# Optimization experiments

Hardware: AMD Instinct MI355X
Metric: run time of the kernel (lower is better)

The kernel has to match this reference:

```python
import jax, jax.numpy as jnp
import numpy as np

N_NODES = 50000
N_EDGES = 1000000
D = 64
L = 3
BN_EPS = 1e-5


def setup_inputs() -> dict:
    key = jax.random.key(0)
    ks = jax.random.split(key, 6)
    x = jax.random.normal(ks[0], (N_NODES, D), dtype=jnp.float32)
    edge_src = jax.random.randint(ks[1], (N_EDGES,), 0, N_NODES)
    edge_dst = jax.random.randint(ks[2], (N_EDGES,), 0, N_NODES)
    edge_weight = jax.random.uniform(ks[3], (N_EDGES,), dtype=jnp.float32)
    W = jax.random.normal(ks[4], (L, D, D), dtype=jnp.float32) * (1.0 / np.sqrt(D))
    b = jnp.zeros((L, D), dtype=jnp.float32)
    prelu_a = jnp.full((L,), 0.25, dtype=jnp.float32)  # torch PReLU default init
    bn_gamma = jnp.ones((L, D), dtype=jnp.float32)
    bn_beta = jnp.zeros((L, D), dtype=jnp.float32)
    return {"x": x, "edge_src": edge_src, "edge_dst": edge_dst,
            "edge_weight": edge_weight, "W": W, "b": b, "prelu_a": prelu_a,
            "bn_gamma": bn_gamma, "bn_beta": bn_beta}


def reference(x, edge_src, edge_dst, edge_weight, W, b, prelu_a, bn_gamma, bn_beta):
    n = x.shape[0]
    h = x
    for i in range(L):
        h_in = h
        # GCNConv (normalize=False): aggregate edge_weight * (h @ W)[src] at dst, + bias
        xw = h @ W[i]                                       # [N, D]
        msg = edge_weight[:, None] * xw[edge_src]            # [E, D] gather
        agg = jax.ops.segment_sum(msg, edge_dst, num_segments=n) + b[i]
        # PReLU (single shared parameter per module)
        h = jnp.where(agg >= 0, agg, prelu_a[i] * agg)
        if i > 0:
            h = h + h_in
        # BatchNorm1d, training-mode batch statistics over nodes
        mean = jnp.mean(h, axis=0)
        var = jnp.mean((h - mean) ** 2, axis=0)  # biased variance, as torch BN
        h = bn_gamma[i] * (h - mean) * jax.lax.rsqrt(var + BN_EPS) + bn_beta[i]
        # dropout p=0.0 -> identity
    return h
```

## Files before the change

### kernel.cpp

```cpp
#include <hip/hip_runtime.h>
#include <hip/hip_fp16.h>

#define N_NODES 50000
#define N_EDGES 1000000
#define D 64
#define L 3
#define BN_EPS 1e-5f
#define NB_SCAN ((N_NODES + 255) / 256)
#define AGG_BLOCKS 1024

__device__ inline void bn_affine(const float* __restrict__ bnsum,
                                 const float* __restrict__ gamma,
                                 const float* __restrict__ beta,
                                 int c, float& sc, float& sh) {
    float mean = bnsum[c] * (1.f / N_NODES);
    float var = fmaf(-mean, mean, bnsum[D + c] * (1.f / N_NODES));
    float inv = rsqrtf(var + BN_EPS);
    sc = gamma[c] * inv;
    sh = fmaf(-mean, sc, beta[c]);
}

__device__ inline float unpack_w(unsigned int m) {
    __half_raw hr;
    hr.x = (unsigned short)(m & 0xffffu);
    __half h = *reinterpret_cast<__half*>(&hr);
    return __half2float(h);
}

__device__ inline float2 unpack_x2(unsigned int q) {
    __half2 h2 = *reinterpret_cast<__half2*>(&q);
    return __half22float2(h2);
}

__device__ inline float2 ntload_f2(const float2* p) {
    unsigned long long u = __builtin_nontemporal_load((const unsigned long long*)p);
    float2 r;
    r.x = __uint_as_float((unsigned int)(u & 0xffffffffull));
    r.y = __uint_as_float((unsigned int)(u >> 32));
    return r;
}

__device__ inline void ntstore_f2(float2* p, float2 v) {
    unsigned long long u =
        ((unsigned long long)__float_as_uint(v.y) << 32) | (unsigned long long)__float_as_uint(v.x);
    __builtin_nontemporal_store(u, (unsigned long long*)p);
}

__global__ void init_kernel(int* __restrict__ counts, float* __restrict__ bnsum) {
    int i = blockIdx.x * blockDim.x + threadIdx.x;
    int stride = gridDim.x * blockDim.x;
    for (int j = i; j < N_NODES; j += stride) counts[j] = 0;
    for (int j = i; j < L * 2 * D; j += stride) bnsum[j] = 0.f;
}

__global__ void count_kernel(const int* __restrict__ dst, int* __restrict__ counts,
                             unsigned short* __restrict__ rank) {
    int i = blockIdx.x * blockDim.x + threadIdx.x;
    int stride = gridDim.x * blockDim.x;
    for (int e = i; e < N_EDGES; e += stride) {
        int r = atomicAdd(&counts[dst[e]], 1);
        rank[e] = (unsigned short)r;
    }
}

__global__ __launch_bounds__(256) void scanA_kernel(const int* __restrict__ counts,
                                                    int* __restrict__ blocksum) {
    __shared__ int buf[256];
    int t = threadIdx.x, b = blockIdx.x;
    int i = b * 256 + t;
    int v = (i < N_NODES) ? counts[i] : 0;
    buf[t] = v;
    __syncthreads();
    for (int off = 128; off > 0; off >>= 1) {
        if (t < off) buf[t] += buf[t + off];
        __syncthreads();
    }
    if (t == 0) blocksum[b] = buf[0];
}

__global__ __launch_bounds__(256) void scanB_kernel(const int* __restrict__ blocksum,
                                                    int* __restrict__ blockoff,
                                                    int* __restrict__ row_ptr) {
    __shared__ int buf[256];
    int t = threadIdx.x;
    int v = (t < NB_SCAN) ? blocksum[t] : 0;
    buf[t] = v;
    __syncthreads();
    for (int off = 1; off < 256; off <<= 1) {
        int u = (t >= off) ? buf[t - off] : 0;
        __syncthreads();
        buf[t] += u;
        __syncthreads();
    }
    if (t < NB_SCAN) blockoff[t] = buf[t] - v;
    if (t == NB_SCAN - 1) row_ptr[N_NODES] = buf[t];
}

__global__ __launch_bounds__(256) void scanC_kernel(const int* __restrict__ counts,
                                                    const int* __restrict__ blockoff,
                                                    int* __restrict__ row_ptr) {
    __shared__ int buf[256];
    int t = threadIdx.x, b = blockIdx.x;
    int i = b * 256 + t;
    int v = (i < N_NODES) ? counts[i] : 0;
    buf[t] = v;
    __syncthreads();
    for (int off = 1; off < 256; off <<= 1) {
        int u = (t >= off) ? buf[t - off] : 0;
        __syncthreads();
        buf[t] += u;
        __syncthreads();
    }
    if (i < N_NODES) row_ptr[i] = blockoff[b] + buf[t] - v;
}

__global__ void fill_kernel(const int* __restrict__ src, const int* __restrict__ dst,
                            const float* __restrict__ w,
                            const unsigned short* __restrict__ rank,
                            const int* __restrict__ row_ptr,
                            unsigned int* __restrict__ em) {
    int i = blockIdx.x * blockDim.x + threadIdx.x;
    int stride = gridDim.x * blockDim.x;
    for (int e = i; e < N_EDGES; e += stride) {
        int d = dst[e];
        int p = row_ptr[d] + (int)rank[e];
        __half h = __float2half_rn(w[e]);
        unsigned short wb = reinterpret_cast<__half_raw*>(&h)->x;
        em[p] = ((unsigned int)src[e] << 16) | (unsigned int)wb;
    }
}

__global__ __launch_bounds__(256) void gemm_kernel(const float* __restrict__ hraw,
                                                   const float* __restrict__ bnsum_p,
                                                   const float* __restrict__ gamma_p,
                                                   const float* __restrict__ beta_p,
                                                   const float* __restrict__ Wl,
                                                   __half* __restrict__ xw) {
    __shared__ float aff[2][D];
    int tid = threadIdx.x, lane = tid & 63, wave = tid >> 6;
    if (tid < D) {
        float sc = 1.f, sh = 0.f;
        if (bnsum_p) bn_affine(bnsum_p, gamma_p, beta_p, tid, sc, sh);
        aff[0][tid] = sc;
        aff[1][tid] = sh;
    }
    __syncthreads();
    float Wreg[D];
    float biasc = 0.f;
#pragma unroll
    for (int k = 0; k < D; k++) {
        float wkc = Wl[k * D + lane];
        biasc = fmaf(aff[1][k], wkc, biasc);
        Wreg[k] = wkc * aff[0][k];
    }
    int gw = blockIdx.x * 4 + wave, nw = gridDim.x * 4;
    for (int v = gw; v < N_NODES; v += nw) {
        const float* hp = hraw + (size_t)__builtin_amdgcn_readfirstlane(v) * D;
        float acc = biasc;
#pragma unroll
        for (int k = 0; k < D; k++) acc = fmaf(hp[k], Wreg[k], acc);
        xw[v * D + lane] = __float2half_rn(acc);
    }
}

__global__ __launch_bounds__(256) void agg_kernel(const uint2* __restrict__ xw,
                                                  const int* __restrict__ row_ptr,
                                                  const unsigned int* __restrict__ em,
                                                  const float* __restrict__ bl,
                                                  const float* __restrict__ pa,
                                                  const float* __restrict__ hraw_prev,
                                                  const float* __restrict__ bnsum_p,
                                                  const float* __restrict__ gamma_p,
                                                  const float* __restrict__ beta_p,
                                                  float* __restrict__ hpre,
                                                  float* __restrict__ bnsum) {
    __shared__ float r1[D], r2[D];
    int tid = threadIdx.x, lane = tid & 63;
    int sub = tid >> 4;
    int fl = lane & 15;
    int srcbase = lane & 48;
    if (tid < D) { r1[tid] = 0.f; r2[tid] = 0.f; }
    __syncthreads();

    float al = pa[0];
    int c0 = 4 * fl;
    float4 bias = ((const float4*)bl)[fl];
    float sc0 = 0, sc1 = 0, sc2 = 0, sc3 = 0, sh0 = 0, sh1 = 0, sh2 = 0, sh3 = 0;
    if (hraw_prev) {
        bn_affine(bnsum_p, gamma_p, beta_p, c0 + 0, sc0, sh0);
        bn_affine(bnsum_p, gamma_p, beta_p, c0 + 1, sc1, sh1);
        bn_affine(bnsum_p, gamma_p, beta_p, c0 + 2, sc2, sh2);
        bn_affine(bnsum_p, gamma_p, beta_p, c0 + 3, sc3, sh3);
    }
    float t1_0 = 0, t1_1 = 0, t1_2 = 0, t1_3 = 0;
    float t2_0 = 0, t2_1 = 0, t2_2 = 0, t2_3 = 0;

    for (int v = blockIdx.x * 16 + sub; v < N_NODES; v += gridDim.x * 16) {
        int e0 = row_ptr[v], e1 = row_ptr[v + 1];
        float a0 = 0, a1 = 0, a2 = 0, a3 = 0, b0 = 0, b1 = 0, b2 = 0, b3 = 0;
        for (int e = e0; e < e1; e += 16) {
            unsigned mo = (e + fl < e1) ? __builtin_nontemporal_load(em + e + fl) : 0u;
            unsigned mj[16];
            uint2 q[16];
#pragma unroll
            for (int j = 0; j < 16; j++) {
                mj[j] = (unsigned)__shfl((int)mo, srcbase + j, 64);
                q[j] = xw[(mj[j] >> 16) * 16 + fl];
            }
#pragma unroll
            for (int j = 0; j < 16; j++) {
                float w = unpack_w(mj[j]);
                float2 f01 = unpack_x2(q[j].x);
                float2 f23 = unpack_x2(q[j].y);
                if (j & 1) {
                    b0 = fmaf(w, f01.x, b0); b1 = fmaf(w, f01.y, b1);
                    b2 = fmaf(w, f23.x, b2); b3 = fmaf(w, f23.y, b3);
                } else {
                    a0 = fmaf(w, f01.x, a0); a1 = fmaf(w, f01.y, a1);
                    a2 = fmaf(w, f23.x, a2); a3 = fmaf(w, f23.y, a3);
                }
            }
        }
        float h0 = a0 + b0 + bias.x;
        float h1 = a1 + b1 + bias.y;
        float h2 = a2 + b2 + bias.z;
        float h3 = a3 + b3 + bias.w;
        h0 = h0 >= 0.f ? h0 : al * h0;
        h1 = h1 >= 0.f ? h1 : al * h1;
        h2 = h2 >= 0.f ? h2 : al * h2;
        h3 = h3 >= 0.f ? h3 : al * h3;
        if (hraw_prev) {
            float2 p01 = ntload_f2((const float2*)hraw_prev + v * 32 + 2 * fl);
            float2 p23 = ntload_f2((const float2*)hraw_prev + v * 32 + 2 * fl + 1);
            h0 = fmaf(p01.x, sc0, h0 + sh0);
            h1 = fmaf(p01.y, sc1, h1 + sh1);
            h2 = fmaf(p23.x, sc2, h2 + sh2);
            h3 = fmaf(p23.y, sc3, h3 + sh3);
        }
        ntstore_f2((float2*)hpre + v * 32 + 2 * fl, make_float2(h0, h1));
        ntstore_f2((float2*)hpre + v * 32 + 2 * fl + 1, make_float2(h2, h3));
        t1_0 += h0; t1_1 += h1; t1_2 += h2; t1_3 += h3;
        t2_0 = fmaf(h0, h0, t2_0);
        t2_1 = fmaf(h1, h1, t2_1);
        t2_2 = fmaf(h2, h2, t2_2);
        t2_3 = fmaf(h3, h3, t2_3);
    }
    atomicAdd(&r1[c0 + 0], t1_0);
    atomicAdd(&r1[c0 + 1], t1_1);
    atomicAdd(&r1[c0 + 2], t1_2);
    atomicAdd(&r1[c0 + 3], t1_3);
    atomicAdd(&r2[c0 + 0], t2_0);
    atomicAdd(&r2[c0 + 1], t2_1);
    atomicAdd(&r2[c0 + 2], t2_2);
    atomicAdd(&r2[c0 + 3], t2_3);
    __syncthreads();
    if (tid < D) {
        atomicAdd(&bnsum[tid], r1[tid]);
        atomicAdd(&bnsum[D + tid], r2[tid]);
    }
}

__global__ __launch_bounds__(256) void bnapply_kernel(const float* __restrict__ hpre,
                                                      const float* __restrict__ bnsum_p,
                                                      const float* __restrict__ gamma_p,
                                                      const float* __restrict__ beta_p,
                                                      float* __restrict__ out) {
    __shared__ float aff[2][D];
    int tid = threadIdx.x;
    if (tid < D) {
        float sc, sh;
        bn_affine(bnsum_p, gamma_p, beta_p, tid, sc, sh);
        aff[0][tid] = sc;
        aff[1][tid] = sh;
    }
    __syncthreads();
    int i = blockIdx.x * blockDim.x + tid;
    int stride = gridDim.x * blockDim.x;
    const int NQ = N_NODES * D / 4;
    for (int j = i; j < NQ; j += stride) {
        float4 hv = ((const float4*)hpre)[j];
        int c = (j * 4) & 63;
        float4 o;
        o.x = fmaf(hv.x, aff[0][c + 0], aff[1][c + 0]);
        o.y = fmaf(hv.y, aff[0][c + 1], aff[1][c + 1]);
        o.z = fmaf(hv.z, aff[0][c + 2], aff[1][c + 2]);
        o.w = fmaf(hv.w, aff[0][c + 3], aff[1][c + 3]);
        ((float4*)out)[j] = o;
    }
}

extern "C" void kernel_launch(void* const* d_in, const int* in_sizes, int n_in,
                              void* d_out, int out_size, void* d_ws, size_t ws_size,
                              hipStream_t stream) {
    const float* x     = (const float*)d_in[0];
    const int*   esrc  = (const int*)d_in[1];
    const int*   edst  = (const int*)d_in[2];
    const float* ew    = (const float*)d_in[3];
    const float* W     = (const float*)d_in[4];
    const float* b     = (const float*)d_in[5];
    const float* pa    = (const float*)d_in[6];
    const float* gamma = (const float*)d_in[7];
    const float* beta  = (const float*)d_in[8];
    float* out = (float*)d_out;

    char* ws = (char*)d_ws;
    size_t off = 0;
    auto alloc = [&](size_t bytes) -> char* {
        char* p = ws + off;
        off = (off + bytes + 255) & ~(size_t)255;
        return p;
    };
    int*            counts   = (int*)alloc((size_t)N_NODES * 4);
    int*            row_ptr  = (int*)alloc((size_t)(N_NODES + 1) * 4);
    int*            blocksum = (int*)alloc((size_t)NB_SCAN * 4);
    int*            blockoff = (int*)alloc((size_t)NB_SCAN * 4);
    unsigned short* rank     = (unsigned short*)alloc((size_t)N_EDGES * 2);
    unsigned int*   em       = (unsigned int*)alloc((size_t)N_EDGES * 4);
    __half*         xw       = (__half*)alloc((size_t)N_NODES * D * 2);
    float*          hpre1    = (float*)alloc((size_t)N_NODES * D * 4);
    float*          bnsum    = (float*)alloc((size_t)L * 2 * D * 4);

    init_kernel<<<256, 256, 0, stream>>>(counts, bnsum);
    count_kernel<<<2048, 256, 0, stream>>>(edst, counts, rank);
    scanA_kernel<<<NB_SCAN, 256, 0, stream>>>(counts, blocksum);
    scanB_kernel<<<1, 256, 0, stream>>>(blocksum, blockoff, row_ptr);
    scanC_kernel<<<NB_SCAN, 256, 0, stream>>>(counts, blockoff, row_ptr);
    fill_kernel<<<2048, 256, 0, stream>>>(esrc, edst, ew, rank, row_ptr, em);

    float* hbuf[L] = {out, hpre1, out};
    for (int i = 0; i < L; i++) {
        const float* hin = (i == 0) ? x : hbuf[i - 1];
        const float* bns = (i == 0) ? nullptr : bnsum + (i - 1) * 2 * D;
        const float* gmp = (i == 0) ? nullptr : gamma + (i - 1) * D;
        const float* btp = (i == 0) ? nullptr : beta + (i - 1) * D;
        gemm_kernel<<<512, 256, 0, stream>>>(hin, bns, gmp, btp, W + (size_t)i * D * D, xw);
        agg_kernel<<<AGG_BLOCKS, 256, 0, stream>>>((const uint2*)xw, row_ptr, em,
                                                   b + i * D, pa + i,
                                                   (i == 0) ? nullptr : hbuf[i - 1],
                                                   bns, gmp, btp,
                                                   hbuf[i], bnsum + i * 2 * D);
    }
    bnapply_kernel<<<2048, 256, 0, stream>>>(hbuf[2], bnsum + 2 * 2 * D,
                                             gamma + 2 * D, beta + 2 * D, out);
}
```

Before: 278.3 us.

## Privatize degree counting per XCD and unroll aggregation to 32 edges

Degree counting now uses a separate counter array per XCD, selected from the hardware XCC id, so atomics stay local to one die's L2. A new kernel turns the per-XCD counts into per-XCD offsets, and the fill pass uses an XCD id packed into the rank field. The aggregation kernel now launches one node per 16-lane group, with no grid-stride loop, and loads 32 edges per iteration to increase gather parallelism. The rank encoding assumes each per-XCD degree fits in 13 bits, and the change adds an extra kernel plus more memory traffic for eight copies of the counts.

Result: slower. 415.5 us (+49.3%).

```diff
diff --git a/kernel.cpp b/kernel.cpp
--- a/kernel.cpp
+++ b/kernel.cpp
@@ -7,7 +7,14 @@
 #define L 3
 #define BN_EPS 1e-5f
 #define NB_SCAN ((N_NODES + 255) / 256)
-#define AGG_BLOCKS 1024
+#define AGG_BLOCKS ((N_NODES + 15) / 16)
+#define NXCD 8
+
+__device__ inline int get_xcc() {
+    int x;
+    asm volatile("s_getreg_b32 %0, hwreg(HW_REG_XCC_ID)" : "=s"(x));
+    return x & (NXCD - 1);
+}
 
 __device__ inline void bn_affine(const float* __restrict__ bnsum,
                                  const float* __restrict__ gamma,
@@ -46,29 +53,37 @@
     __builtin_nontemporal_store(u, (unsigned long long*)p);
 }
 
-__global__ void init_kernel(int* __restrict__ counts, float* __restrict__ bnsum) {
+__global__ void init_kernel(int* __restrict__ counts8, float* __restrict__ bnsum) {
     int i = blockIdx.x * blockDim.x + threadIdx.x;
     int stride = gridDim.x * blockDim.x;
-    for (int j = i; j < N_NODES; j += stride) counts[j] = 0;
+    for (int j = i; j < NXCD * N_NODES; j += stride) counts8[j] = 0;
     for (int j = i; j < L * 2 * D; j += stride) bnsum[j] = 0.f;
 }
 
-__global__ void count_kernel(const int* __restrict__ dst, int* __restrict__ counts,
-                             unsigned short* __restrict__ rank) {
+__global__ void count_kernel(const int* __restrict__ dst, int* __restrict__ counts8,
+                             unsigned short* __restrict__ rankx) {
+    int xcd = get_xcc();
+    int* mycnt = counts8 + (size_t)xcd * N_NODES;
     int i = blockIdx.x * blockDim.x + threadIdx.x;
     int stride = gridDim.x * blockDim.x;
     for (int e = i; e < N_EDGES; e += stride) {
-        int r = atomicAdd(&counts[dst[e]], 1);
-        rank[e] = (unsigned short)r;
-    }
-}
-
-__global__ __launch_bounds__(256) void scanA_kernel(const int* __restrict__ counts,
+        int r = atomicAdd(&mycnt[dst[e]], 1);
+        rankx[e] = (unsigned short)(r | (xcd << 13));
+    }
+}
+
+__global__ __launch_bounds__(256) void scanA_kernel(const int* __restrict__ counts8,
+                                                    int* __restrict__ counts,
                                                     int* __restrict__ blocksum) {
     __shared__ int buf[256];
     int t = threadIdx.x, b = blockIdx.x;
     int i = b * 256 + t;
-    int v = (i < N_NODES) ? counts[i] : 0;
+    int v = 0;
+    if (i < N_NODES) {
+#pragma unroll
+        for (int x = 0; x < NXCD; x++) v += counts8[(size_t)x * N_NODES + i];
+        counts[i] = v;
+    }
     buf[t] = v;
     __syncthreads();
     for (int off = 128; off > 0; off >>= 1) {
@@ -114,16 +129,31 @@
     if (i < N_NODES) row_ptr[i] = blockoff[b] + buf[t] - v;
 }
 
+__global__ __launch_bounds__(256) void offs8_kernel(const int* __restrict__ counts8,
+                                                    const int* __restrict__ row_ptr,
+                                                    int* __restrict__ offs8) {
+    int i = blockIdx.x * blockDim.x + threadIdx.x;
+    if (i < N_NODES) {
+        int base = row_ptr[i];
+#pragma unroll
+        for (int x = 0; x < NXCD; x++) {
+            offs8[(size_t)x * N_NODES + i] = base;
+            base += counts8[(size_t)x * N_NODES + i];
+        }
+    }
+}
+
 __global__ void fill_kernel(const int* __restrict__ src, const int* __restrict__ dst,
                             const float* __restrict__ w,
-                            const unsigned short* __restrict__ rank,
-                            const int* __restrict__ row_ptr,
+                            const unsigned short* __restrict__ rankx,
+                            const int* __restrict__ offs8,
                             unsigned int* __restrict__ em) {
     int i = blockIdx.x * blockDim.x + threadIdx.x;
     int stride = gridDim.x * blockDim.x;
     for (int e = i; e < N_EDGES; e += stride) {
         int d = dst[e];
-        int p = row_ptr[d] + (int)rank[e];
+        unsigned rx = rankx[e];
+        int p = offs8[(size_t)(rx >> 13) * N_NODES + d] + (int)(rx & 0x1fffu);
         __half h = __float2half_rn(w[e]);
         unsigned short wb = reinterpret_cast<__half_raw*>(&h)->x;
         em[p] = ((unsigned int)src[e] << 16) | (unsigned int)wb;
@@ -195,21 +225,28 @@
     float t1_0 = 0, t1_1 = 0, t1_2 = 0, t1_3 = 0;
     float t2_0 = 0, t2_1 = 0, t2_2 = 0, t2_3 = 0;
 
-    for (int v = blockIdx.x * 16 + sub; v < N_NODES; v += gridDim.x * 16) {
+    int v = blockIdx.x * 16 + sub;
+    if (v < N_NODES) {
         int e0 = row_ptr[v], e1 = row_ptr[v + 1];
         float a0 = 0, a1 = 0, a2 = 0, a3 = 0, b0 = 0, b1 = 0, b2 = 0, b3 = 0;
-        for (int e = e0; e < e1; e += 16) {
-            unsigned mo = (e + fl < e1) ? __builtin_nontemporal_load(em + e + fl) : 0u;
-            unsigned mj[16];
-            uint2 q[16];
+        for (int e = e0; e < e1; e += 32) {
+            unsigned mlo = (e + fl < e1) ? __builtin_nontemporal_load(em + e + fl) : 0u;
+            unsigned mhi = (e + 16 + fl < e1) ? __builtin_nontemporal_load(em + e + 16 + fl) : 0u;
+            uint2 q[32];
 #pragma unroll
             for (int j = 0; j < 16; j++) {
-                mj[j] = (unsigned)__shfl((int)mo, srcbase + j, 64);
-                q[j] = xw[(mj[j] >> 16) * 16 + fl];
+                unsigned m = (unsigned)__shfl((int)mlo, srcbase + j, 64);
+                q[j] = xw[(m >> 16) * 16 + fl];
             }
 #pragma unroll
             for (int j = 0; j < 16; j++) {
-                float w = unpack_w(mj[j]);
+                unsigned m = (unsigned)__shfl((int)mhi, srcbase + j, 64);
+                q[16 + j] = xw[(m >> 16) * 16 + fl];
+            }
+#pragma unroll
+            for (int j = 0; j < 32; j++) {
+                unsigned m = (unsigned)__shfl((int)(j < 16 ? mlo : mhi), srcbase + (j & 15), 64);
+                float w = unpack_w(m);
                 float2 f01 = unpack_x2(q[j].x);
                 float2 f23 = unpack_x2(q[j].y);
                 if (j & 1) {
@@ -239,11 +276,8 @@
         }
         ntstore_f2((float2*)hpre + v * 32 + 2 * fl, make_float2(h0, h1));
         ntstore_f2((float2*)hpre + v * 32 + 2 * fl + 1, make_float2(h2, h3));
-        t1_0 += h0; t1_1 += h1; t1_2 += h2; t1_3 += h3;
-        t2_0 = fmaf(h0, h0, t2_0);
-        t2_1 = fmaf(h1, h1, t2_1);
-        t2_2 = fmaf(h2, h2, t2_2);
-        t2_3 = fmaf(h3, h3, t2_3);
+        t1_0 = h0; t1_1 = h1; t1_2 = h2; t1_3 = h3;
+        t2_0 = h0 * h0; t2_1 = h1 * h1; t2_2 = h2 * h2; t2_3 = h3 * h3;
     }
     atomicAdd(&r1[c0 + 0], t1_0);
     atomicAdd(&r1[c0 + 1], t1_1);
@@ -310,22 +344,25 @@
         off = (off + bytes + 255) & ~(size_t)255;
         return p;
     };
+    int*            counts8  = (int*)alloc((size_t)NXCD * N_NODES * 4);
     int*            counts   = (int*)alloc((size_t)N_NODES * 4);
     int*            row_ptr  = (int*)alloc((size_t)(N_NODES + 1) * 4);
+    int*            offs8    = (int*)alloc((size_t)NXCD * N_NODES * 4);
     int*            blocksum = (int*)alloc((size_t)NB_SCAN * 4);
     int*            blockoff = (int*)alloc((size_t)NB_SCAN * 4);
-    unsigned short* rank     = (unsigned short*)alloc((size_t)N_EDGES * 2);
+    unsigned short* rankx    = (unsigned short*)alloc((size_t)N_EDGES * 2);
     unsigned int*   em       = (unsigned int*)alloc((size_t)N_EDGES * 4);
     __half*         xw       = (__half*)alloc((size_t)N_NODES * D * 2);
     float*          hpre1    = (float*)alloc((size_t)N_NODES * D * 4);
     float*          bnsum    = (float*)alloc((size_t)L * 2 * D * 4);
 
-    init_kernel<<<256, 256, 0, stream>>>(counts, bnsum);
-    count_kernel<<<2048, 256, 0, stream>>>(edst, counts, rank);
-    scanA_kernel<<<NB_SCAN, 256, 0, stream>>>(counts, blocksum);
+    init_kernel<<<512, 256, 0, stream>>>(counts8, bnsum);
+    count_kernel<<<2048, 256, 0, stream>>>(edst, counts8, rankx);
+    scanA_kernel<<<NB_SCAN, 256, 0, stream>>>(counts8, counts, blocksum);
     scanB_kernel<<<1, 256, 0, stream>>>(blocksum, blockoff, row_ptr);
     scanC_kernel<<<NB_SCAN, 256, 0, stream>>>(counts, blockoff, row_ptr);
-    fill_kernel<<<2048, 256, 0, stream>>>(esrc, edst, ew, rank, row_ptr, em);
+    offs8_kernel<<<NB_SCAN, 256, 0, stream>>>(counts8, row_ptr, offs8);
+    fill_kernel<<<2048, 256, 0, stream>>>(esrc, edst, ew, rankx, offs8, em);
 
     float* hbuf[L] = {out, hpre1, out};
     for (int i = 0; i < L; i++) {
```
